# Optimization experiments

Measured on AMD Instinct MI355X. Metric: run time of the kernel, lower is better.

## Reference

```python
import jax, jax.numpy as jnp
import numpy as np
from jax import lax

SCORE_THRESHOLD = 0.5
IOU_THRESHOLD = 0.5
IMG_SIZE = 640.0
SPLITTER_THRESHOLD = 0.0
N = 4096


def setup_inputs() -> dict:
    key = jax.random.key(0)
    # raw RT-DETR output: [1, N, 5] = (cx, cy, w, h, person_conf), all in [0, 1]
    rtdetr_raw_out = jax.random.uniform(key, (1, N, 5), dtype=jnp.float32)
    return {"rtdetr_raw_out": rtdetr_raw_out}


def _iou_matrix(boxes):
    # boxes: [N, 4] in xyxy. Returns [N, N] pairwise IoU.
    x1, y1, x2, y2 = boxes[:, 0], boxes[:, 1], boxes[:, 2], boxes[:, 3]
    area = (x2 - x1) * (y2 - y1)  # [N]
    ix1 = jnp.maximum(x1[:, None], x1[None, :])
    iy1 = jnp.maximum(y1[:, None], y1[None, :])
    ix2 = jnp.minimum(x2[:, None], x2[None, :])
    iy2 = jnp.minimum(y2[:, None], y2[None, :])
    iw = jnp.clip(ix2 - ix1, 0.0)
    ih = jnp.clip(iy2 - iy1, 0.0)
    inter = iw * ih
    union = area[:, None] + area[None, :] - inter
    return inter / jnp.maximum(union, 1e-9)


def reference(rtdetr_raw_out):
    raw = rtdetr_raw_out[0]  # squeeze(0) -> [N, 5]
    conf = raw[:, 4]
    # splitter: keep boxes with conf > 0.0 (expressed as a mask for fixed shapes)
    valid = conf > SPLITTER_THRESHOLD
    # cxcywh scaled to pixel coords, then converted to xyxy
    cxcywh = raw[:, :4] * IMG_SIZE
    cx, cy, w, h = cxcywh[:, 0], cxcywh[:, 1], cxcywh[:, 2], cxcywh[:, 3]
    xyxy = jnp.stack([cx - w * 0.5, cy - h * 0.5, cx + w * 0.5, cy + h * 0.5], axis=1)
    # NMS score filter: conf >= score_threshold
    valid = valid & (conf >= SCORE_THRESHOLD)
    # sort by score descending; invalid boxes sink to the bottom with -inf keys
    sort_key = jnp.where(valid, conf, -jnp.inf)
    order = jnp.argsort(-sort_key)
    boxes_s = xyxy[order]          # [N, 4]
    conf_s = conf[order]           # [N]
    valid_s = valid[order]         # [N]
    iou = _iou_matrix(boxes_s)     # [N, N]
    idx = jnp.arange(N)

    def body(i, keep):
        keep_i = keep[i]
        # suppress any lower-ranked box with IoU > threshold to a kept box i
        sup = (iou[i] > IOU_THRESHOLD) & keep_i & (idx > i)
        return keep & (~sup)

    keep = lax.fori_loop(0, N, body, valid_s)
    boxes_and_scores = jnp.concatenate([boxes_s, conf_s[:, None]], axis=1)  # [N, 5]
    # fixed-shape equivalent of boolean-gather: suppressed/invalid rows zeroed
    return boxes_and_scores * keep[:, None].astype(boxes_and_scores.dtype)
```

## Files before the change

### kernel.cpp

```cpp
#include <hip/hip_runtime.h>
#include <stdint.h>

#define NBOX 4096
#define IMG 640.0f

typedef unsigned long long u64;


__global__ __launch_bounds__(256) void k_rank(const float* __restrict__ raw,
                                              int* __restrict__ rank_partial, int* __restrict__ Mp) {
    const int bi = blockIdx.x, bj = blockIdx.y;
    const int t = threadIdx.x;
    const int i = bi * 256 + t;
    if (bi == 0 && bj == 0 && t == 0) *Mp = 0;
    __shared__ float cj[256];
    cj[t] = raw[(bj * 256 + t) * 5 + 4];
    __syncthreads();

    const float ci = raw[i * 5 + 4];
    const int jbase = bj * 256;
    int rank = 0;
    const float4* c4 = reinterpret_cast<const float4*>(cj);
#pragma unroll 4
    for (int j4 = 0; j4 < 64; ++j4) {
        float4 c = c4[j4];
        int j = jbase + j4 * 4;
        rank += (c.x > ci || (c.x == ci && (j + 0) < i)) ? 1 : 0;
        rank += (c.y > ci || (c.y == ci && (j + 1) < i)) ? 1 : 0;
        rank += (c.z > ci || (c.z == ci && (j + 2) < i)) ? 1 : 0;
        rank += (c.w > ci || (c.w == ci && (j + 3) < i)) ? 1 : 0;
    }
    rank_partial[bj * NBOX + i] = rank;
}

__global__ __launch_bounds__(256) void k_scatter(const float* __restrict__ raw,
                                                 const int* __restrict__ rank_partial,
                                                 float* __restrict__ sx1, float* __restrict__ sy1,
                                                 float* __restrict__ sx2, float* __restrict__ sy2,
                                                 float* __restrict__ sconf, int* __restrict__ Mp) {
    const int i = blockIdx.x * 256 + threadIdx.x;
    const float ci = raw[i * 5 + 4];
    const bool vi = (ci >= 0.5f);

    int rank = 0;
#pragma unroll
    for (int k = 0; k < 16; ++k) rank += rank_partial[k * NBOX + i];

    u64 bal = __ballot(vi);
    if ((threadIdx.x & 63) == 0) atomicAdd(Mp, (int)__popcll(bal));

    if (vi) {
        float cx = __fmul_rn(raw[i * 5 + 0], IMG);
        float cy = __fmul_rn(raw[i * 5 + 1], IMG);
        float w  = __fmul_rn(raw[i * 5 + 2], IMG);
        float h  = __fmul_rn(raw[i * 5 + 3], IMG);
        float hw = __fmul_rn(w, 0.5f);
        float hh = __fmul_rn(h, 0.5f);
        sx1[rank]   = __fsub_rn(cx, hw);
        sy1[rank]   = __fsub_rn(cy, hh);
        sx2[rank]   = __fadd_rn(cx, hw);
        sy2[rank]   = __fadd_rn(cy, hh);
        sconf[rank] = ci;
    }
}

__global__ __launch_bounds__(256) void k_mask(const float* __restrict__ sx1, const float* __restrict__ sy1,
                                              const float* __restrict__ sx2, const float* __restrict__ sy2,
                                              const int* __restrict__ Mp,
                                              u64* __restrict__ mask, u64* __restrict__ diagT) {
    const int w = blockIdx.y;
    const int r = blockIdx.x * 256 + threadIdx.x;
    const int t = threadIdx.x;
    const int M = *Mp;

    __shared__ float cx1[64], cy1[64], cx2[64], cy2[64], car[64];
    if (t < 64) {
        int j = (w << 6) + t;
        float a1 = sx1[j], b1 = sy1[j], a2 = sx2[j], b2 = sy2[j];
        cx1[t] = a1; cy1[t] = b1; cx2[t] = a2; cy2[t] = b2;
        car[t] = __fmul_rn(__fsub_rn(a2, a1), __fsub_rn(b2, b1));
    }
    __syncthreads();

    u64 bits = 0ULL;
    if (r < M) {
        const float x1 = sx1[r], y1 = sy1[r], x2 = sx2[r], y2 = sy2[r];
        const float area_i = __fmul_rn(__fsub_rn(x2, x1), __fsub_rn(y2, y1));
        const int bmax = min(64, M - (w << 6));
        const int bmin = max(0, r + 1 - (w << 6));
        for (int b = bmin; b < bmax; ++b) {
            float xx1 = fmaxf(x1, cx1[b]);
            float yy1 = fmaxf(y1, cy1[b]);
            float xx2 = fminf(x2, cx2[b]);
            float yy2 = fminf(y2, cy2[b]);
            float iw = fmaxf(__fsub_rn(xx2, xx1), 0.0f);
            float ih = fmaxf(__fsub_rn(yy2, yy1), 0.0f);
            float inter = __fmul_rn(iw, ih);
            float uni = __fsub_rn(__fadd_rn(area_i, car[b]), inter);
            float iou = __fdiv_rn(inter, fmaxf(uni, 1e-9f));
            if (iou > 0.5f) bits |= (1ULL << b);
        }
        mask[((size_t)r << 6) + w] = bits;
    }

    if ((r >> 6) == w) {
        const int myj = r & 63;
        u64 colv = 0ULL;
#pragma unroll 1
        for (int j = 0; j < 64; ++j) {
            u64 bb = __ballot((int)((bits >> j) & 1ULL));
            if (myj == j) colv = bb;
        }
        diagT[(w << 6) + myj] = colv;
    }
}

#define DEPTH 4
#define LOOKAHEAD 3

#define GLDS(gp, lp)  __builtin_amdgcn_global_load_lds( \
    (const __attribute__((address_space(1))) void*)(gp), \
    (__attribute__((address_space(3))) void*)(lp), 16, 0, 0)

__global__ __launch_bounds__(576) void k_scan(const int* __restrict__ Mp,
                                              const u64* __restrict__ mask,
                                              const u64* __restrict__ diagT,
                                              u64* __restrict__ keepw) {
    __shared__ u64 tile[DEPTH][64 * 64];
    const int tid = threadIdx.x;
    const int wave = tid >> 6;
    const int lane = tid & 63;
    const int M = *Mp;
    const int nblk = (M + 63) >> 6;
    if (nblk == 0) return;

    if (wave == 0) {
        __builtin_amdgcn_s_setprio(1);
        u64 remv = 0ULL;
        u64 col = diagT[lane];
        __builtin_amdgcn_s_barrier();
        for (int b = 0; b < nblk; ++b) {
            __builtin_amdgcn_sched_barrier(0);
            u64 ncol = (b + 1 < nblk) ? diagT[((b + 1) << 6) + lane] : 0ULL;

            u64 rb = __shfl(remv, b);
            bool a0 = (((rb >> lane) & 1ULL) == 0ULL) && (((b << 6) + lane) < M);
            u64 alive = __ballot(a0);

            u64 kb = 0ULL;
            while (alive) {
                int i = __builtin_ctzll(alive);
                alive &= alive - 1;
                kb |= (1ULL << i);
                u64 sup = __ballot((int)((col >> i) & 1ULL));
                alive &= ~sup;
            }
            if (lane == 0) keepw[b] = kb;

            const u64* tb = tile[b & (DEPTH - 1)];
            u64 acc = 0ULL, t = kb;
            while (t) {
                int i0 = __builtin_ctzll(t); t &= t - 1;
                int i1 = -1;
                if (t) { i1 = __builtin_ctzll(t); t &= t - 1; }
                u64 v0 = tb[(i0 << 6) + lane];
                u64 v1 = (i1 >= 0) ? tb[(i1 << 6) + lane] : 0ULL;
                acc |= v0 | v1;
            }
            remv |= acc;
            col = ncol;
            __builtin_amdgcn_s_barrier();
        }
    } else {
        const char* mb = (const char*)mask;
        const int w1 = wave - 1;
        char* lbase = (char*)&tile[0][0];

        for (int blk = 0; blk < LOOKAHEAD && blk < nblk; ++blk) {
            const char* g = mb + ((size_t)blk << 15) + (w1 << 12) + (lane << 4);
            char* l = lbase + ((size_t)(blk & (DEPTH - 1)) << 15) + (w1 << 12);
#pragma unroll
            for (int c = 0; c < 4; ++c) GLDS(g + (c << 10), l + (c << 10));
        }
        asm volatile("s_waitcnt vmcnt(0)" ::: "memory");
        __builtin_amdgcn_s_barrier();

        for (int b = 0; b < nblk; ++b) {
            __builtin_amdgcn_sched_barrier(0);
            const int nb = b + LOOKAHEAD;
            if (nb < nblk) {
                const char* g = mb + ((size_t)nb << 15) + (w1 << 12) + (lane << 4);
                char* l = lbase + ((size_t)(nb & (DEPTH - 1)) << 15) + (w1 << 12);
#pragma unroll
                for (int c = 0; c < 4; ++c) GLDS(g + (c << 10), l + (c << 10));
                asm volatile("s_waitcnt vmcnt(8)" ::: "memory");
            } else {
                asm volatile("s_waitcnt vmcnt(0)" ::: "memory");
            }
            __builtin_amdgcn_s_barrier();
        }
    }
}

__global__ __launch_bounds__(256) void k_out(const float* __restrict__ sx1, const float* __restrict__ sy1,
                                             const float* __restrict__ sx2, const float* __restrict__ sy2,
                                             const float* __restrict__ sconf,
                                             const int* __restrict__ Mp,
                                             const u64* __restrict__ keepw,
                                             float* __restrict__ out) {
    const int g = blockIdx.x * 256 + threadIdx.x;
    if (g >= NBOX * 5) return;
    const int r = g / 5;
    const int c = g - r * 5;
    const int M = *Mp;
    bool kept = false;
    if (r < M) kept = ((keepw[r >> 6] >> (r & 63)) & 1ULL) != 0ULL;
    float v = 0.0f;
    if (kept) {
        const float* arr = (c == 0) ? sx1 : (c == 1) ? sy1 : (c == 2) ? sx2 : (c == 3) ? sy2 : sconf;
        v = arr[r];
    }
    out[g] = v;
}

extern "C" void kernel_launch(void* const* d_in, const int* in_sizes, int n_in,
                              void* d_out, int out_size, void* d_ws, size_t ws_size,
                              hipStream_t stream) {
    const float* raw = (const float*)d_in[0];
    char* ws = (char*)d_ws;
    float* sx1 = (float*)(ws + 0);
    float* sy1 = (float*)(ws + 16384);
    float* sx2 = (float*)(ws + 32768);
    float* sy2 = (float*)(ws + 49152);
    float* sconf = (float*)(ws + 65536);
    int* Mp = (int*)(ws + 81920);
    u64* keepw = (u64*)(ws + 82432);
    u64* diagT = (u64*)(ws + 86016);
    u64* mask = (u64*)(ws + 131072);
    int* rank_partial = (int*)(ws + 2228224);
    float* out = (float*)d_out;

    k_rank<<<dim3(16, 16), dim3(256), 0, stream>>>(raw, rank_partial, Mp);
    k_scatter<<<dim3(16), dim3(256), 0, stream>>>(raw, rank_partial, sx1, sy1, sx2, sy2, sconf, Mp);
    k_mask<<<dim3(16, 64), dim3(256), 0, stream>>>(sx1, sy1, sx2, sy2, Mp, mask, diagT);
    k_scan<<<dim3(1), dim3(576), 0, stream>>>(Mp, mask, diagT, keepw);
    k_out<<<dim3(80), dim3(256), 0, stream>>>(sx1, sy1, sx2, sy2, sconf, Mp, keepw, out);
}
```

Measured before the change: 93.51 us.

## Restructure NMS scan: readlane row masks, lag-one remv accumulation by helper waves

```diff
diff --git a/kernel.cpp b/kernel.cpp
--- a/kernel.cpp
+++ b/kernel.cpp
@@ -5,6 +5,7 @@
 #define IMG 640.0f
 
 typedef unsigned long long u64;
+typedef unsigned int u32;
 
 
 __global__ __launch_bounds__(256) void k_rank(const float* __restrict__ raw,
@@ -67,7 +68,7 @@
 __global__ __launch_bounds__(256) void k_mask(const float* __restrict__ sx1, const float* __restrict__ sy1,
                                               const float* __restrict__ sx2, const float* __restrict__ sy2,
                                               const int* __restrict__ Mp,
-                                              u64* __restrict__ mask, u64* __restrict__ diagT) {
+                                              u64* __restrict__ mask, u64* __restrict__ diagR) {
     const int w = blockIdx.y;
     const int r = blockIdx.x * 256 + threadIdx.x;
     const int t = threadIdx.x;
@@ -103,30 +104,15 @@
         mask[((size_t)r << 6) + w] = bits;
     }
 
-    if ((r >> 6) == w) {
-        const int myj = r & 63;
-        u64 colv = 0ULL;
-#pragma unroll 1
-        for (int j = 0; j < 64; ++j) {
-            u64 bb = __ballot((int)((bits >> j) & 1ULL));
-            if (myj == j) colv = bb;
-        }
-        diagT[(w << 6) + myj] = colv;
-    }
-}
-
-#define DEPTH 4
-#define LOOKAHEAD 3
-
-#define GLDS(gp, lp)  __builtin_amdgcn_global_load_lds( \
-    (const __attribute__((address_space(1))) void*)(gp), \
-    (__attribute__((address_space(3))) void*)(lp), 16, 0, 0)
+    if ((r >> 6) == w) diagR[r] = bits;
+}
 
 __global__ __launch_bounds__(576) void k_scan(const int* __restrict__ Mp,
                                               const u64* __restrict__ mask,
-                                              const u64* __restrict__ diagT,
+                                              const u64* __restrict__ diagR,
                                               u64* __restrict__ keepw) {
-    __shared__ u64 tile[DEPTH][64 * 64];
+    __shared__ u64 remvArr[64];
+    __shared__ u64 kbArr[64];
     const int tid = threadIdx.x;
     const int wave = tid >> 6;
     const int lane = tid & 63;
@@ -134,70 +120,77 @@
     const int nblk = (M + 63) >> 6;
     if (nblk == 0) return;
 
+    if (tid < 64) remvArr[tid] = 0ULL;
+
     if (wave == 0) {
         __builtin_amdgcn_s_setprio(1);
-        u64 remv = 0ULL;
-        u64 col = diagT[lane];
-        __builtin_amdgcn_s_barrier();
+        u64 rv = diagR[lane];
+        u32 rlo = (u32)rv, rhi = (u32)(rv >> 32);
+        u64 colv = (nblk > 1) ? mask[((size_t)lane << 6) + 1] : 0ULL;
+        u64 carry = 0ULL;
+
         for (int b = 0; b < nblk; ++b) {
-            __builtin_amdgcn_sched_barrier(0);
-            u64 ncol = (b + 1 < nblk) ? diagT[((b + 1) << 6) + lane] : 0ULL;
-
-            u64 rb = __shfl(remv, b);
-            bool a0 = (((rb >> lane) & 1ULL) == 0ULL) && (((b << 6) + lane) < M);
-            u64 alive = __ballot(a0);
-
+            u64 rb = remvArr[b];
+            const int rem = M - (b << 6);
+            const u64 valid = (rem >= 64) ? ~0ULL : ((1ULL << rem) - 1ULL);
+            u64 alive = valid & ~(rb | carry);
             u64 kb = 0ULL;
             while (alive) {
                 int i = __builtin_ctzll(alive);
                 alive &= alive - 1;
                 kb |= (1ULL << i);
-                u64 sup = __ballot((int)((col >> i) & 1ULL));
-                alive &= ~sup;
+                u32 lo = __builtin_amdgcn_readlane(rlo, i);
+                u32 hi = __builtin_amdgcn_readlane(rhi, i);
+                alive &= ~(((u64)hi << 32) | (u64)lo);
             }
-            if (lane == 0) keepw[b] = kb;
-
-            const u64* tb = tile[b & (DEPTH - 1)];
-            u64 acc = 0ULL, t = kb;
-            while (t) {
-                int i0 = __builtin_ctzll(t); t &= t - 1;
-                int i1 = -1;
-                if (t) { i1 = __builtin_ctzll(t); t &= t - 1; }
-                u64 v0 = tb[(i0 << 6) + lane];
-                u64 v1 = (i1 >= 0) ? tb[(i1 << 6) + lane] : 0ULL;
-                acc |= v0 | v1;
+            if (lane == 0) { kbArr[b] = kb; keepw[b] = kb; }
+
+            u64 nc = ((kb >> lane) & 1ULL) ? colv : 0ULL;
+            nc |= __shfl_xor(nc, 1);
+            nc |= __shfl_xor(nc, 2);
+            nc |= __shfl_xor(nc, 4);
+            nc |= __shfl_xor(nc, 8);
+            nc |= __shfl_xor(nc, 16);
+            nc |= __shfl_xor(nc, 32);
+            carry = nc;
+
+            if (b + 1 < nblk) {
+                u64 nrv = diagR[((b + 1) << 6) + lane];
+                rlo = (u32)nrv; rhi = (u32)(nrv >> 32);
+                colv = (b + 2 < nblk)
+                     ? mask[(((size_t)(b + 1) << 6) + lane) * 64 + (b + 2)]
+                     : 0ULL;
             }
-            remv |= acc;
-            col = ncol;
+            asm volatile("s_waitcnt lgkmcnt(0)" ::: "memory");
             __builtin_amdgcn_s_barrier();
+            __builtin_amdgcn_sched_barrier(0);
         }
     } else {
-        const char* mb = (const char*)mask;
         const int w1 = wave - 1;
-        char* lbase = (char*)&tile[0][0];
-
-        for (int blk = 0; blk < LOOKAHEAD && blk < nblk; ++blk) {
-            const char* g = mb + ((size_t)blk << 15) + (w1 << 12) + (lane << 4);
-            char* l = lbase + ((size_t)(blk & (DEPTH - 1)) << 15) + (w1 << 12);
+        const int slot = tid & 7;
+        const int chunk = (tid >> 3) & 7;
+        for (int b = 0; b < nblk; ++b) {
+            if (b >= 1) {
+                const u64 kb = kbArr[b - 1];
+                const int W = b + 1 + (w1 << 3) + slot;
+                if (kb != 0ULL && W < 64) {
+                    const u64* rowbase = mask + ((size_t)(b - 1) << 12);
+                    u64 acc = 0ULL;
 #pragma unroll
-            for (int c = 0; c < 4; ++c) GLDS(g + (c << 10), l + (c << 10));
-        }
-        asm volatile("s_waitcnt vmcnt(0)" ::: "memory");
-        __builtin_amdgcn_s_barrier();
-
-        for (int b = 0; b < nblk; ++b) {
+                    for (int k = 0; k < 8; ++k) {
+                        const int r = chunk + (k << 3);
+                        u64 v = rowbase[((size_t)r << 6) + W];
+                        acc |= (((kb >> r) & 1ULL) ? v : 0ULL);
+                    }
+                    acc |= __shfl_xor(acc, 8);
+                    acc |= __shfl_xor(acc, 16);
+                    acc |= __shfl_xor(acc, 32);
+                    if (chunk == 0) remvArr[W] |= acc;
+                }
+            }
+            asm volatile("s_waitcnt lgkmcnt(0)" ::: "memory");
+            __builtin_amdgcn_s_barrier();
             __builtin_amdgcn_sched_barrier(0);
-            const int nb = b + LOOKAHEAD;
-            if (nb < nblk) {
-                const char* g = mb + ((size_t)nb << 15) + (w1 << 12) + (lane << 4);
-                char* l = lbase + ((size_t)(nb & (DEPTH - 1)) << 15) + (w1 << 12);
-#pragma unroll
-                for (int c = 0; c < 4; ++c) GLDS(g + (c << 10), l + (c << 10));
-                asm volatile("s_waitcnt vmcnt(8)" ::: "memory");
-            } else {
-                asm volatile("s_waitcnt vmcnt(0)" ::: "memory");
-            }
-            __builtin_amdgcn_s_barrier();
         }
     }
 }
@@ -235,14 +228,14 @@
     float* sconf = (float*)(ws + 65536);
     int* Mp = (int*)(ws + 81920);
     u64* keepw = (u64*)(ws + 82432);
-    u64* diagT = (u64*)(ws + 86016);
+    u64* diagR = (u64*)(ws + 86016);
     u64* mask = (u64*)(ws + 131072);
     int* rank_partial = (int*)(ws + 2228224);
     float* out = (float*)d_out;
 
     k_rank<<<dim3(16, 16), dim3(256), 0, stream>>>(raw, rank_partial, Mp);
     k_scatter<<<dim3(16), dim3(256), 0, stream>>>(raw, rank_partial, sx1, sy1, sx2, sy2, sconf, Mp);
-    k_mask<<<dim3(16, 64), dim3(256), 0, stream>>>(sx1, sy1, sx2, sy2, Mp, mask, diagT);
-    k_scan<<<dim3(1), dim3(576), 0, stream>>>(Mp, mask, diagT, keepw);
+    k_mask<<<dim3(16, 64), dim3(256), 0, stream>>>(sx1, sy1, sx2, sy2, Mp, mask, diagR);
+    k_scan<<<dim3(1), dim3(576), 0, stream>>>(Mp, mask, diagR, keepw);
     k_out<<<dim3(80), dim3(256), 0, stream>>>(sx1, sy1, sx2, sy2, sconf, Mp, keepw, out);
 }
```

After: 91.62 us. 1.02x faster.
